# Performance work log

Measured on AMD Instinct MI355X. Metric: run time of the kernel, lower is better.

Reference implementation:

```python
import jax, jax.numpy as jnp
import numpy as np

SIZES = (1, 2, 4, 8)
C_IN = 64
KC = C_IN // 8      # key_channels = out_channels // 8 = 8
VC = C_IN           # value_channels = out_channels = 64
N_STAGES = len(SIZES)


def setup_inputs() -> dict:
    key = jax.random.key(0)
    ks = jax.random.split(key, 16)
    N, C, H, W = 1, C_IN, 64, 64
    inp = {
        "x1": jax.random.normal(ks[0], (N, C, H, W), jnp.float32),
        "x2": jax.random.normal(ks[1], (N, C, H, W), jnp.float32),
        # per-stage 1x1 conv weights (stacked over the 4 PAM stages)
        "Wq": jax.random.normal(ks[2], (N_STAGES, KC, C), jnp.float32) * 0.02,
        "bq": jnp.zeros((N_STAGES, KC), jnp.float32),
        "gammaq": 1.0 + jax.random.normal(ks[3], (N_STAGES, KC), jnp.float32) * 0.02,
        "betaq": jnp.zeros((N_STAGES, KC), jnp.float32),
        "Wk": jax.random.normal(ks[4], (N_STAGES, KC, C), jnp.float32) * 0.02,
        "bk": jnp.zeros((N_STAGES, KC), jnp.float32),
        "gammak": 1.0 + jax.random.normal(ks[5], (N_STAGES, KC), jnp.float32) * 0.02,
        "betak": jnp.zeros((N_STAGES, KC), jnp.float32),
        "Wv": jax.random.normal(ks[6], (N_STAGES, VC, C), jnp.float32) * 0.02,
        "bv": jnp.zeros((N_STAGES, VC), jnp.float32),
        # final 1x1 conv: in = C * n_stages, out = C, no bias
        "Wo": jax.random.normal(ks[7], (C, VC * N_STAGES), jnp.float32) * 0.02,
    }
    return inp


def _pam_block(x, Wq, bq, gq, betq, Wk, bk, gk, betk, Wv, bv, scale):
    # x: [N, C, H, 2W] (two images concatenated along width)
    N, C, H, W2 = x.shape
    w = W2 // 2
    kc = Wq.shape[0]

    def proj(W, b):  # 1x1 conv
        return jnp.einsum('nchw,kc->nkhw', x, W) + b[:, None, None]

    # BatchNorm (inference form: zero running mean / unit variance) folded to affine
    q = gq[:, None, None] * proj(Wq, bq) + betq[:, None, None]
    k = gk[:, None, None] * proj(Wk, bk) + betk[:, None, None]
    v = proj(Wv, bv)

    hl, wl = H // scale, w // scale

    def to_blocks(t):
        ch = t.shape[1]
        # stack left/right halves on a trailing axis: [N, ch, H, w, 2]
        t = jnp.stack([t[..., :w], t[..., w:]], axis=-1)
        # split into scale x scale spatial blocks -> [N, s*s, ch, hl*wl*2]
        t = t.reshape(N, ch, scale, hl, scale, wl, 2)
        t = t.transpose(0, 2, 4, 1, 3, 5, 6)
        return t.reshape(N, scale * scale, ch, hl * wl * 2)

    qb, kb, vb = to_blocks(q), to_blocks(k), to_blocks(v)

    sim = jnp.einsum('nbkp,nbkq->nbpq', qb, kb) * (kc ** -0.5)
    att = jax.nn.softmax(sim, axis=-1)
    # context = V @ att^T : ctx[c,p] = sum_q v[c,q] * att[p,q]
    ctx = jnp.einsum('nbcq,nbpq->nbcp', vb, att)

    Cv = Wv.shape[0]
    ctx = ctx.reshape(N, scale, scale, Cv, hl, wl, 2)
    ctx = ctx.transpose(0, 3, 1, 4, 2, 5, 6).reshape(N, Cv, H, w, 2)
    # re-concatenate the two halves along width -> [N, Cv, H, 2w]
    return jnp.concatenate([ctx[..., 0], ctx[..., 1]], axis=3)


def reference(x1, x2, Wq, bq, gammaq, betaq, Wk, bk, gammak, betak, Wv, bv, Wo):
    h_w = x1.shape[3]
    x = jnp.concatenate([x1, x2], axis=3)  # [N, C, H, 2W]
    priors = [
        _pam_block(x, Wq[i], bq[i], gammaq[i], betaq[i],
                   Wk[i], bk[i], gammak[i], betak[i],
                   Wv[i], bv[i], SIZES[i])
        for i in range(N_STAGES)
    ]
    cat = jnp.concatenate(priors, axis=1)  # [N, 4C, H, 2W]
    out = jnp.einsum('ndhw,od->nohw', cat, Wo)  # final 1x1 conv, no bias
    return out[:, :, :, :h_w], out[:, :, :, h_w:]


if __name__ == '__main__':
    o1, o2 = reference(**setup_inputs())
    print(o1.shape, o2.shape)
```

## Files before the change

### kernel.cpp

```cpp
#include <hip/hip_runtime.h>


typedef _Float16 f16x8 __attribute__((ext_vector_type(8)));
typedef float f32x16 __attribute__((ext_vector_type(16)));
typedef short bf16x8 __attribute__((ext_vector_type(8)));

__device__ __forceinline__ unsigned short f2bf(float f){
    union{float f;unsigned int i;}v; v.f=f;
    unsigned int r = v.i + 0x7fffu + ((v.i>>16)&1u);
    return (unsigned short)(r>>16);
}
__device__ __forceinline__ unsigned short f2h(float f){
    union{_Float16 h; unsigned short u;}v; v.h = (_Float16)f; return v.u;
}
__device__ __forceinline__ unsigned pack2h(float a, float b){
    auto pk = __builtin_amdgcn_cvt_pkrtz(a, b);
    unsigned u; __builtin_memcpy(&u, &pk, 4); return u;
}
__device__ __forceinline__ float exp2fast(float x){ return __builtin_amdgcn_exp2f(x); }
__device__ __forceinline__ int rfl(int x){ return __builtin_amdgcn_readfirstlane(x); }

#define QMUL 0.5100697233f

__global__ __launch_bounds__(256) void proj_all_kernel(
    const float* __restrict__ x1, const float* __restrict__ x2,
    const float* __restrict__ Wq, const float* __restrict__ bq,
    const float* __restrict__ gq, const float* __restrict__ beq,
    const float* __restrict__ Wk, const float* __restrict__ bk,
    const float* __restrict__ gk, const float* __restrict__ bek,
    const float* __restrict__ Wv, const float* __restrict__ bv,
    unsigned short* __restrict__ Qb, unsigned short* __restrict__ Kb,
    unsigned short* __restrict__ Vf)
{
    __shared__ __align__(16) float xs[64][68];
    __shared__ __align__(16) unsigned vqk[64][8];
    __shared__ __align__(16) unsigned short vv[64][64];

    const int wg = blockIdx.x, st = wg >> 8, rr = wg & 255;
    const int chunk = rr >> 1, cgrp = rr & 1;
    const int lgP = 13 - 2*st, Pm1 = (1<<lgP) - 1;
    const int hb = 6 - st, wlm = (1<<hb) - 1;
    const int t = threadIdx.x;
    const int gp0 = chunk*64;
    const int blk = gp0 >> lgP, p0 = gp0 & Pm1;
    const int si = blk >> st, sj = blk & ((1<<st)-1);
    const int hwbase = ((si<<hb)<<6) | (sj<<hb);

    for (int idx = t; idx < 4096; idx += 256) {
        int c = idx >> 6, g = idx & 63;
        int p = p0 + g, half = p & 1, pw = p >> 1;
        int hw = hwbase | ((pw>>hb)<<6) | (pw & wlm);
        xs[g][c] = (half ? x2 : x1)[c*4096 + hw];
    }
    __syncthreads();

    const int px = t & 63, wv = t >> 6;
    float xr[64];
    #pragma unroll
    for (int q4 = 0; q4 < 16; ++q4)
        *(float4*)&xr[q4*4] = *(const float4*)&xs[px][q4*4];

#define VRANGE(LO,HI)                                              \
    for (int ch = (LO); ch < (HI); ++ch) {                         \
        const int cu = rfl(st*64 + ch);                            \
        const float* wp = Wv + cu*64;                              \
        float d = bv[cu];                                          \
        _Pragma("unroll")                                          \
        for (int k = 0; k < 64; ++k) d += wp[k]*xr[k];             \
        vv[ch][px] = f2h(d);                                       \
    }
#define KPROJ(CH,DST)                                              \
    {   const int cu = rfl(st*8 + (CH));                           \
        const float* wp = Wk + cu*64;                              \
        float d = 0.f;                                             \
        _Pragma("unroll")                                          \
        for (int k = 0; k < 64; ++k) d += wp[k]*xr[k];             \
        float gm = gk[cu];                                         \
        (DST) = gm*(d + bk[cu]) + bek[cu]; }

    if (cgrp == 0) {
        if (wv == 0) {
            float qv8[8];
            for (int ch = 0; ch < 8; ++ch) {
                const int cu = rfl(st*8 + ch);
                const float* wp = Wq + cu*64;
                float d = 0.f;
                #pragma unroll
                for (int k = 0; k < 64; ++k) d += wp[k]*xr[k];
                float gm = gq[cu];
                qv8[ch] = (gm*(d + bq[cu]) + beq[cu])*QMUL;
            }
            #pragma unroll
            for (int i = 0; i < 4; ++i) vqk[px][i] = pack2h(qv8[2*i], qv8[2*i+1]);
            float k0v, k1v; KPROJ(0, k0v) KPROJ(1, k1v)
            vqk[px][4] = pack2h(k0v, k1v);
        } else if (wv == 1) {
            float ka, kb2;
            KPROJ(2, ka) KPROJ(3, kb2) vqk[px][5] = pack2h(ka, kb2);
            KPROJ(4, ka) KPROJ(5, kb2) vqk[px][6] = pack2h(ka, kb2);
            KPROJ(6, ka) KPROJ(7, kb2) vqk[px][7] = pack2h(ka, kb2);
            VRANGE(0, 4)
        } else if (wv == 2) { VRANGE(4, 14) }
        else               { VRANGE(14, 24) }
    } else {
        if      (wv == 0) { VRANGE(24, 34) }
        else if (wv == 1) { VRANGE(34, 44) }
        else if (wv == 2) { VRANGE(44, 54) }
        else              { VRANGE(54, 64) }
    }
#undef VRANGE
#undef KPROJ
    __syncthreads();

    unsigned short* Vst = Vf + st*524288 + (blk << (lgP+6));
    if (cgrp == 0) {
        if (t < 64) {
            *(uint4*)(Qb + st*65536 + (gp0 + t)*8) = *(const uint4*)&vqk[t][0];
        } else if (t < 128) {
            int p2 = t - 64;
            *(uint4*)(Kb + st*65536 + (gp0 + p2)*8) = *(const uint4*)&vqk[p2][4];
        }
        if (t < 192) {
            int ch = t >> 3, q = t & 7;
            int kb = q >> 1, lhi = q & 1;
            unsigned short tmp[8];
            #pragma unroll
            for (int u = 0; u < 8; ++u) {
                int s = q*8 + u;
                tmp[u] = vv[ch][((s&1)<<5) | (s>>1)];
            }
            *(uint4*)(Vst + p0*64 + kb*1024 + (lhi*32 + ch)*8) = *(const uint4*)tmp;
        }
    } else {
        for (int task = t; task < 320; task += 256) {
            int ch = 24 + (task >> 3), q = task & 7;
            int kb = q >> 1, lhi = q & 1;
            int b = (ch >= 32) ? 1 : 0, l31 = ch & 31;
            unsigned short tmp[8];
            #pragma unroll
            for (int u = 0; u < 8; ++u) {
                int s = q*8 + u;
                tmp[u] = vv[ch][((s&1)<<5) | (s>>1)];
            }
            *(uint4*)(Vst + p0*64 + kb*1024 + b*512 + (lhi*32 + l31)*8) = *(const uint4*)tmp;
        }
    }
}

__global__ __launch_bounds__(512) void attn_kernel(
    const unsigned short* __restrict__ Qb, const unsigned short* __restrict__ Kb,
    const unsigned short* __restrict__ Vf,
    float* __restrict__ PART, float* __restrict__ LPART)
{
    __shared__ __align__(16) unsigned short Ps[8][2432];

    const int wg = blockIdx.x;
    const int t = threadIdx.x, lane = t & 63, wv = t >> 6;
    const int l31 = lane & 31, lhi = lane >> 5;

    int st, qt, slot, kbase, nkw;
    if (wg < 512)       { st=0; qt=wg>>1;  slot=wg&1;
                          kbase=(wg&1)*4096 + wv*512; nkw=512; }
    else if (wg < 1024) { int r=wg-512;  st=1; qt=r>>1; slot=2+(r&1);
                          kbase=(r&1)*1024 + wv*128;  nkw=128; }
    else if (wg < 1280) { st=2; qt=wg-1024; slot=4; kbase=wv*64; nkw=64; }
    else                { st=3; qt=wg-1280; slot=5; kbase=wv*64;
                          nkw=(wv<2)?64:0; }

    const int lgP = 13 - 2*st, P = 1 << lgP;
    const int blk = qt >> (lgP - 5);
    const int q0  = (qt & ((P>>5)-1)) * 32;

    const unsigned short* Qg = Qb + st*65536 + blk*P*8;
    const unsigned short* Kg = Kb + st*65536 + blk*P*8;
    const unsigned short* Vg = Vf + st*524288 + blk*P*64;

    f16x8 qa;
    #pragma unroll
    for (int j = 0; j < 8; ++j) qa[j] = (_Float16)0.f;
    if (lane < 32) qa = *(const f16x8*)(Qg + (q0 + l31)*8);

    f32x16 acc0, acc1;
    #pragma unroll
    for (int r = 0; r < 16; ++r) { acc0[r] = 0.f; acc1[r] = 0.f; }
    float rowsum[16];
    #pragma unroll
    for (int r = 0; r < 16; ++r) rowsum[r] = 0.f;

    unsigned short* Pw = Ps[wv];
    unsigned* Pw32 = (unsigned*)Pw;
    for (int k0 = kbase; k0 < kbase + nkw; k0 += 64) {
        f16x8 kb0 = *(const f16x8*)(Kg + (k0 + l31)*8);
        f16x8 kb1 = *(const f16x8*)(Kg + (k0 + 32 + l31)*8);
        f32x16 S0, S1;
        #pragma unroll
        for (int r = 0; r < 16; ++r) { S0[r] = 0.f; S1[r] = 0.f; }
        S0 = __builtin_amdgcn_mfma_f32_32x32x16_f16(qa, kb0, S0, 0, 0, 0);
        S1 = __builtin_amdgcn_mfma_f32_32x32x16_f16(qa, kb1, S1, 0, 0, 0);

        #pragma unroll
        for (int r = 0; r < 16; ++r) {
            float p0 = exp2fast(S0[r]);
            float p1 = exp2fast(S1[r]);
            rowsum[r] += p0 + p1;
            int qrow = (r&3) + 8*(r>>2) + 4*lhi;
            Pw32[qrow*38 + l31] = pack2h(p0, p1);
        }

        #pragma unroll
        for (int kc = 0; kc < 4; ++kc) {
            f16x8 pa  = *(const f16x8*)(Pw + l31*76 + kc*16 + 8*lhi);
            const unsigned short* vbase = Vg + (k0 + kc*16)*64;
            f16x8 vb0 = *(const f16x8*)(vbase + lane*8);
            f16x8 vb1 = *(const f16x8*)(vbase + 512 + lane*8);
            acc0 = __builtin_amdgcn_mfma_f32_32x32x16_f16(pa, vb0, acc0, 0, 0, 0);
            acc1 = __builtin_amdgcn_mfma_f32_32x32x16_f16(pa, vb1, acc1, 0, 0, 0);
        }
    }

    float* SC = (float*)Pw;
    #pragma unroll
    for (int r = 0; r < 16; ++r) {
        int qrow = (r&3) + 8*(r>>2) + 4*lhi;
        SC[qrow*33 + l31] = rowsum[r];
    }
    float lsum_reg = 0.f;
    if (lane < 32) {
        #pragma unroll 8
        for (int j = 0; j < 32; ++j) lsum_reg += SC[l31*33 + j];
    }

    float* BB = (float*)&Ps[0][0];
    float* Lm = BB + 8192;
    __syncthreads();
    if (wv < 4) {
        float* B = BB + wv*2048;
        #pragma unroll
        for (int r = 0; r < 16; ++r) {
            int qrow = (r&3) + 8*(r>>2) + 4*lhi;
            B[qrow*64 + l31]      = acc0[r];
            B[qrow*64 + 32 + l31] = acc1[r];
        }
        if (lane < 32) Lm[wv*32 + l31] = lsum_reg;
    }
    __syncthreads();
    if (wv >= 4) {
        float* B = BB + (wv-4)*2048;
        #pragma unroll
        for (int r = 0; r < 16; ++r) {
            int qrow = (r&3) + 8*(r>>2) + 4*lhi;
            B[qrow*64 + l31]      += acc0[r];
            B[qrow*64 + 32 + l31] += acc1[r];
        }
        if (lane < 32) Lm[(wv-4)*32 + l31] += lsum_reg;
    }
    __syncthreads();

    float4* Pslab4 = (float4*)(PART + slot*524288 + qt*2048);
    const float4* B4 = (const float4*)BB;
    {
        float4 a = B4[t], b = B4[t+512], c = B4[t+1024], d = B4[t+1536];
        Pslab4[t] = float4{a.x+b.x+c.x+d.x, a.y+b.y+c.y+d.y,
                           a.z+b.z+c.z+d.z, a.w+b.w+c.w+d.w};
    }
    if (t < 32)
        LPART[slot*8192 + qt*32 + t] = Lm[t] + Lm[32+t] + Lm[64+t] + Lm[96+t];
}

__global__ __launch_bounds__(256) void normconv_kernel(
    const float* __restrict__ PART, const float* __restrict__ LPART,
    const float* __restrict__ Wo, float* __restrict__ out)
{
    __shared__ __align__(16) unsigned short csb[32][264];
    __shared__ __align__(16) unsigned short wof[16384];
    __shared__ float voutf[64][33];
    __shared__ float linv[4][32];
    __shared__ int gpar[4][32];
    const int t = threadIdx.x;
    const int px0 = blockIdx.x * 32;

    {
        int oc = t >> 2, d0 = (t & 3) * 64;
        for (int b = 0; b < 8; ++b) {
            int d = d0 + b*8;
            float4 w0 = *(const float4*)(Wo + oc*256 + d);
            float4 w1 = *(const float4*)(Wo + oc*256 + d + 4);
            unsigned short tmp[8];
            tmp[0]=f2bf(w0.x); tmp[1]=f2bf(w0.y); tmp[2]=f2bf(w0.z); tmp[3]=f2bf(w0.w);
            tmp[4]=f2bf(w1.x); tmp[5]=f2bf(w1.y); tmp[6]=f2bf(w1.z); tmp[7]=f2bf(w1.w);
            *(uint4*)&wof[(d>>3)*512 + oc*8] = *(const uint4*)tmp;
        }
    }
    if (t < 128) {
        const int s0tab[4] = {0,2,4,5};
        const int sctab[4] = {2,2,1,1};
        int stt = t >> 5, i = t & 31;
        int pix = px0 + i;
        int half = pix >> 12, hw = pix & 4095;
        int h = hw >> 6, w = hw & 63;
        int hb = 6 - stt, wlm = (1<<hb)-1;
        int si = h >> hb, sj = w >> hb, hi = h & wlm, wi = w & wlm;
        int blk = (si << stt) | sj;
        int p = (((hi << hb) | wi) << 1) | half;
        int gp = blk*(8192>>(2*stt)) + p;
        gpar[stt][i] = gp;
        int s0 = s0tab[stt];
        float l = LPART[s0*8192 + gp];
        if (sctab[stt] == 2) l += LPART[(s0+1)*8192 + gp];
        linv[stt][i] = 1.f / l;
    }
    __syncthreads();

    {
        const int s0tab[4] = {0,2,4,5};
        int gpx = t >> 3, cvg = (t & 7) * 8;
        for (int stt = 0; stt < 4; ++stt) {
            int gp = gpar[stt][gpx];
            const float* p = PART + s0tab[stt]*524288
                           + (gp>>5)*2048 + (gp&31)*64 + cvg;
            float4 a = *(const float4*)p;
            float4 b = *(const float4*)(p + 4);
            if (stt < 2) {
                float4 a2 = *(const float4*)(p + 524288);
                float4 b2 = *(const float4*)(p + 524288 + 4);
                a.x+=a2.x; a.y+=a2.y; a.z+=a2.z; a.w+=a2.w;
                b.x+=b2.x; b.y+=b2.y; b.z+=b2.z; b.w+=b2.w;
            }
            float li = linv[stt][gpx];
            unsigned short tmp[8];
            tmp[0]=f2bf(a.x*li); tmp[1]=f2bf(a.y*li); tmp[2]=f2bf(a.z*li); tmp[3]=f2bf(a.w*li);
            tmp[4]=f2bf(b.x*li); tmp[5]=f2bf(b.y*li); tmp[6]=f2bf(b.z*li); tmp[7]=f2bf(b.w*li);
            *(uint4*)&csb[gpx][stt*64 + cvg] = *(const uint4*)tmp;
        }
    }
    __syncthreads();

    const int lane = t & 63, wvv = t >> 6;
    const int l31 = lane & 31, lhi = lane >> 5;
    const int nh = wvv & 1, kh = wvv >> 1;
    f32x16 acc;
    #pragma unroll
    for (int r = 0; r < 16; ++r) acc[r] = 0.f;
    #pragma unroll
    for (int s = 0; s < 8; ++s) {
        int dg = kh*16 + s*2 + lhi;
        bf16x8 a = *(const bf16x8*)&csb[l31][kh*128 + s*16 + 8*lhi];
        bf16x8 b = *(const bf16x8*)&wof[dg*512 + (nh*32 + l31)*8];
        acc = __builtin_amdgcn_mfma_f32_32x32x16_bf16(a, b, acc, 0, 0, 0);
    }
    if (kh == 0) {
        #pragma unroll
        for (int r = 0; r < 16; ++r)
            voutf[nh*32 + l31][(r&3) + 8*(r>>2) + 4*lhi] = acc[r];
    }
    __syncthreads();
    if (kh == 1) {
        #pragma unroll
        for (int r = 0; r < 16; ++r)
            voutf[nh*32 + l31][(r&3) + 8*(r>>2) + 4*lhi] += acc[r];
    }
    __syncthreads();

    const int half = px0 >> 12, hw0 = px0 & 4095;
    float* obase = out + half*262144 + hw0;
    #pragma unroll
    for (int r = 0; r < 8; ++r) {
        int idx = t + r*256;
        int oc = idx >> 5, pxi = idx & 31;
        obase[oc*4096 + pxi] = voutf[oc][pxi];
    }
}

extern "C" void kernel_launch(void* const* d_in, const int* in_sizes, int n_in,
                              void* d_out, int out_size, void* d_ws, size_t ws_size,
                              hipStream_t stream)
{
    (void)out_size; (void)ws_size;
    const float *x1, *x2, *Wq, *bq, *gq, *beq, *Wk, *bk, *gk, *bek, *Wv, *bv, *Wo;

    if (n_in >= 13 && in_sizes[0] == 2048) {
        Wk  = (const float*)d_in[0];  Wo  = (const float*)d_in[1];
        Wq  = (const float*)d_in[2];  Wv  = (const float*)d_in[3];
        bek = (const float*)d_in[4];  beq = (const float*)d_in[5];
        bk  = (const float*)d_in[6];  bq  = (const float*)d_in[7];
        bv  = (const float*)d_in[8];  gk  = (const float*)d_in[9];
        gq  = (const float*)d_in[10];
        x1  = (const float*)d_in[11]; x2  = (const float*)d_in[12];
    } else {
        x1  = (const float*)d_in[0];  x2  = (const float*)d_in[1];
        Wq  = (const float*)d_in[2];  bq  = (const float*)d_in[3];
        gq  = (const float*)d_in[4];  beq = (const float*)d_in[5];
        Wk  = (const float*)d_in[6];  bk  = (const float*)d_in[7];
        gk  = (const float*)d_in[8];  bek = (const float*)d_in[9];
        Wv  = (const float*)d_in[10]; bv  = (const float*)d_in[11];
        Wo  = (const float*)d_in[12];
    }

    unsigned short* Qb = (unsigned short*)d_ws;
    unsigned short* Kb = Qb + 262144;
    unsigned short* Vf = Kb + 262144;
    float* PART  = (float*)d_ws + 1310720;
    float* LPART = PART + 3145728;

    proj_all_kernel<<<1024, 256, 0, stream>>>(x1,x2,Wq,bq,gq,beq,Wk,bk,gk,bek,Wv,bv,Qb,Kb,Vf);
    attn_kernel<<<1536, 512, 0, stream>>>(Qb,Kb,Vf,PART,LPART);
    normconv_kernel<<<256, 256, 0, stream>>>(PART, LPART, Wo, (float*)d_out);
}
```

Baseline: 147.8 us.

## Compute transposed scores so probabilities stay in registers for PV MFMA

Swaps the MFMA operand order so the score tile is K×Q instead of Q×K. Each lane's accumulator values then line up with the B-operand layout of the following P·V MFMA, so probabilities are packed straight into registers. This removes the per-iteration LDS write and read of the probability tile and the 32-way row-sum reduction through shared memory. The cost is a different zero-padding pattern for the K operand and a restructured shared-memory layout.

```diff
diff --git a/kernel.cpp b/kernel.cpp
--- a/kernel.cpp
+++ b/kernel.cpp
@@ -152,7 +152,9 @@
     const unsigned short* __restrict__ Vf,
     float* __restrict__ PART, float* __restrict__ LPART)
 {
-    __shared__ __align__(16) unsigned short Ps[8][2432];
+    __shared__ __align__(16) float BB[8192];
+    __shared__ float Lm[128];
+    __shared__ float SCm[8][64];
 
     const int wg = blockIdx.x;
     const int t = threadIdx.x, lane = t & 63, wv = t >> 6;
@@ -175,64 +177,56 @@
     const unsigned short* Kg = Kb + st*65536 + blk*P*8;
     const unsigned short* Vg = Vf + st*524288 + blk*P*64;
 
-    f16x8 qa;
-    #pragma unroll
-    for (int j = 0; j < 8; ++j) qa[j] = (_Float16)0.f;
-    if (lane < 32) qa = *(const f16x8*)(Qg + (q0 + l31)*8);
+    f16x8 qb = *(const f16x8*)(Qg + (q0 + l31)*8);
 
     f32x16 acc0, acc1;
     #pragma unroll
     for (int r = 0; r < 16; ++r) { acc0[r] = 0.f; acc1[r] = 0.f; }
-    float rowsum[16];
-    #pragma unroll
-    for (int r = 0; r < 16; ++r) rowsum[r] = 0.f;
-
-    unsigned short* Pw = Ps[wv];
-    unsigned* Pw32 = (unsigned*)Pw;
+    float rs[4];
+    #pragma unroll
+    for (int r = 0; r < 4; ++r) rs[r] = 0.f;
+
     for (int k0 = kbase; k0 < kbase + nkw; k0 += 64) {
-        f16x8 kb0 = *(const f16x8*)(Kg + (k0 + l31)*8);
-        f16x8 kb1 = *(const f16x8*)(Kg + (k0 + 32 + l31)*8);
+        f16x8 ka0, ka1;
+        #pragma unroll
+        for (int j = 0; j < 8; ++j) { ka0[j] = (_Float16)0.f; ka1[j] = (_Float16)0.f; }
+        if (lane < 32) {
+            ka0 = *(const f16x8*)(Kg + (k0 + l31)*8);
+            ka1 = *(const f16x8*)(Kg + (k0 + 32 + l31)*8);
+        }
         f32x16 S0, S1;
         #pragma unroll
         for (int r = 0; r < 16; ++r) { S0[r] = 0.f; S1[r] = 0.f; }
-        S0 = __builtin_amdgcn_mfma_f32_32x32x16_f16(qa, kb0, S0, 0, 0, 0);
-        S1 = __builtin_amdgcn_mfma_f32_32x32x16_f16(qa, kb1, S1, 0, 0, 0);
-
+        S0 = __builtin_amdgcn_mfma_f32_32x32x16_f16(ka0, qb, S0, 0, 0, 0);
+        S1 = __builtin_amdgcn_mfma_f32_32x32x16_f16(ka1, qb, S1, 0, 0, 0);
+
+        unsigned pw[16];
         #pragma unroll
         for (int r = 0; r < 16; ++r) {
-            float p0 = exp2fast(S0[r]);
-            float p1 = exp2fast(S1[r]);
-            rowsum[r] += p0 + p1;
-            int qrow = (r&3) + 8*(r>>2) + 4*lhi;
-            Pw32[qrow*38 + l31] = pack2h(p0, p1);
+            float e0 = exp2fast(S0[r]);
+            float e1 = exp2fast(S1[r]);
+            rs[r & 3] += e0 + e1;
+            pw[r] = pack2h(e0, e1);
         }
 
         #pragma unroll
         for (int kc = 0; kc < 4; ++kc) {
-            f16x8 pa  = *(const f16x8*)(Pw + l31*76 + kc*16 + 8*lhi);
+            f16x8 pb;
+            __builtin_memcpy(&pb, &pw[kc*4], 16);
             const unsigned short* vbase = Vg + (k0 + kc*16)*64;
             f16x8 vb0 = *(const f16x8*)(vbase + lane*8);
             f16x8 vb1 = *(const f16x8*)(vbase + 512 + lane*8);
-            acc0 = __builtin_amdgcn_mfma_f32_32x32x16_f16(pa, vb0, acc0, 0, 0, 0);
-            acc1 = __builtin_amdgcn_mfma_f32_32x32x16_f16(pa, vb1, acc1, 0, 0, 0);
-        }
-    }
-
-    float* SC = (float*)Pw;
-    #pragma unroll
-    for (int r = 0; r < 16; ++r) {
-        int qrow = (r&3) + 8*(r>>2) + 4*lhi;
-        SC[qrow*33 + l31] = rowsum[r];
-    }
+            acc0 = __builtin_amdgcn_mfma_f32_32x32x16_f16(pb, vb0, acc0, 0, 0, 0);
+            acc1 = __builtin_amdgcn_mfma_f32_32x32x16_f16(pb, vb1, acc1, 0, 0, 0);
+        }
+    }
+
+    float lsum = rs[0] + rs[1] + rs[2] + rs[3];
+    SCm[wv][lhi*32 + l31] = lsum;
+    __syncthreads();
     float lsum_reg = 0.f;
-    if (lane < 32) {
-        #pragma unroll 8
-        for (int j = 0; j < 32; ++j) lsum_reg += SC[l31*33 + j];
-    }
-
-    float* BB = (float*)&Ps[0][0];
-    float* Lm = BB + 8192;
-    __syncthreads();
+    if (lane < 32) lsum_reg = SCm[wv][l31] + SCm[wv][32 + l31];
+
     if (wv < 4) {
         float* B = BB + wv*2048;
         #pragma unroll
```

Result: faster. 132.4 us (-10.4%).
